# Optimization experiments

Hardware: AMD Instinct MI355X
Metric: run time of the kernel (lower is better)

Reference implementation:

```python
import jax, jax.numpy as jnp
import numpy as np

KAPPA = 10000.0
B_CONST = 0.5


def pe_matrix(L, dim):
    # pe[j,i] = sin(j/kappa^(i/dim)) for even i, cos(j/kappa^((i-1)/dim)) for odd i
    j = jnp.arange(L, dtype=jnp.float32)[:, None]
    i = jnp.arange(dim, dtype=jnp.float32)[None, :]
    even = (jnp.arange(dim) % 2 == 0)[None, :]
    expo = jnp.where(even, i, i - 1.0) / dim
    ang = j / (KAPPA ** expo)
    return jnp.where(even, jnp.sin(ang), jnp.cos(ang))  # [L, dim]


def setup_inputs() -> dict:
    key = jax.random.key(0)
    ks = jax.random.split(key, 6)
    B, N, L, d, n = 4, 8, 1024, 256, 3
    theta = jax.random.normal(ks[0], (B, N, L, d), dtype=jnp.float32)
    xi = jax.random.normal(ks[1], (B, N, L, n), dtype=jnp.float32)
    edge_attr = jax.random.normal(ks[2], (B, L, N * (N - 1) * 2), dtype=jnp.float32)
    s = 1.0 / np.sqrt(d)
    Wq = jax.random.normal(ks[3], (d, d), dtype=jnp.float32) * s
    Wk = jax.random.normal(ks[4], (d, d), dtype=jnp.float32) * s
    Wv = jax.random.normal(ks[5], (d, d), dtype=jnp.float32) * s
    return {"theta": theta, "xi": xi, "edge_attr": edge_attr, "Wq": Wq, "Wk": Wk, "Wv": Wv}


def reference(theta, xi, edge_attr, Wq, Wk, Wv):
    B, N, L, d = theta.shape
    n = xi.shape[-1]
    # positional encoding (dropout in eval mode = identity)
    theta = theta + pe_matrix(L, d)
    xi = xi + pe_matrix(L, n)
    edge_attr = edge_attr + pe_matrix(L, N * (N - 1) * 2)[None]

    causal = jnp.triu(jnp.ones((L, L), dtype=bool), 1)  # True above diagonal
    neg_inf = jnp.float32(-jnp.inf)

    # feature path: standard causal scaled-dot-product attention
    q = jnp.einsum('bnld,ed->bnle', theta, Wq)
    k = jnp.einsum('bnld,ed->bnle', theta, Wk)
    v = jnp.einsum('bnld,ed->bnle', theta, Wv)
    scores = jnp.einsum('bnqd,bnkd->bnqk', q, k) / jnp.sqrt(jnp.float32(d))
    scores = jnp.where(causal, neg_inf, scores)
    h_out = jnp.einsum('bnqk,bnkd->bnqd', jax.nn.softmax(scores, axis=-1), v)

    # equivariant path: pairwise squared-distance attention
    D = xi[:, :, :, None, :] - xi[:, :, None, :, :]  # [B,N,L,L,n]
    sq = jnp.sum(D * D, axis=-1)                     # [B,N,L,L]
    sq = jnp.where(causal, neg_inf, sq)
    beta = jax.nn.softmax(sq, axis=-1)
    mbeta = beta * (1.0 - jnp.eye(L, dtype=beta.dtype))  # zero the diagonal
    second = B_CONST * jnp.einsum('bnqk,bnkc->bnqc', mbeta, xi)
    third = B_CONST * jnp.sum(mbeta, axis=-1, keepdims=True) * xi
    x_out = xi + second - third

    return h_out, x_out, edge_attr
```

## Files before the change

kernel.cpp:

```cpp
#include <hip/hip_runtime.h>
#include <math.h>

#define L    1024
#define D    256
#define NCH  3
#define HEADS 32
#define EDIM 112
#define BATCH 4

typedef __bf16 bf8_t __attribute__((ext_vector_type(8)));
typedef float  f4_t  __attribute__((ext_vector_type(4)));

typedef __attribute__((address_space(1))) const void GVC;
typedef __attribute__((address_space(3))) void LDSV;

__device__ inline unsigned short f2bf(float x) {
    unsigned u = __float_as_uint(x);
    u += 0x7FFFu + ((u >> 16) & 1u);
    return (unsigned short)(u >> 16);
}
__device__ inline float bf2f(unsigned short h) {
    return __uint_as_float(((unsigned)h) << 16);
}

__global__ void prep_kernel(const float* __restrict__ edge, const float* __restrict__ xi,
                            const float* __restrict__ Wq, const float* __restrict__ Wk,
                            const float* __restrict__ Wv,
                            float* __restrict__ pe_d, float* __restrict__ eout,
                            float* __restrict__ xsb, unsigned short* __restrict__ whb)
{
    int idx = blockIdx.x * blockDim.x + threadIdx.x;
    if (idx < L * D) {
        int l = idx >> 8, i = idx & (D - 1);
        float expo = (float)(i & ~1) * (1.0f / (float)D);
        float ang = (float)l * __powf(10000.0f, -expo);
        pe_d[idx] = (i & 1) ? cosf(ang) : sinf(ang);
    } else if (idx < L * D + BATCH * L * EDIM) {
        int j = idx - L * D;
        int i = j % EDIM;
        int l = (j / EDIM) % L;
        float expo = (float)(i & ~1) * (1.0f / (float)EDIM);
        float ang = (float)l * __powf(10000.0f, -expo);
        eout[j] = edge[j] + ((i & 1) ? cosf(ang) : sinf(ang));
    } else if (idx < L * D + BATCH * L * EDIM + HEADS * L * NCH) {
        int j = idx - (L * D + BATCH * L * EDIM);
        int c = j % 3;
        int l = (j / 3) & (L - 1);
        float ang = (c == 2) ? (float)l * 0.0021544347f : (float)l;
        float pe = (c == 1) ? cosf(ang) : sinf(ang);
        xsb[j] = xi[j] + pe;
    } else {
        int j = idx - (L * D + BATCH * L * EDIM + HEADS * L * NCH);
        if (j < 3 * 8192) {
            int wsel = j >> 13;
            int t = j & 8191;
            int g = t >> 9, u = (t >> 4) & 31, rr = t & 15;
            const float* W = (wsel == 0) ? Wq : (wsel == 1) ? Wk : Wv;
            const float4* s = reinterpret_cast<const float4*>(&W[(size_t)(g * 16 + rr) * D + u * 8]);
            float4 a = s[0], b = s[1];
            float x[8] = {a.x, a.y, a.z, a.w, b.x, b.y, b.z, b.w};
            union { unsigned short us[8]; float4 f4; } hv;
            #pragma unroll
            for (int q = 0; q < 8; q++) hv.us[q] = f2bf(x[q]);
            *reinterpret_cast<float4*>(&whb[(size_t)wsel * 65536 + g * 4096 + u * 128 + rr * 8]) = hv.f4;
        }
    }
}

__global__ __launch_bounds__(512) void qkv_mfma(
    const float* __restrict__ theta, const float* __restrict__ pe_d,
    const unsigned short* __restrict__ whb,
    unsigned short* __restrict__ qh, unsigned short* __restrict__ ql,
    unsigned short* __restrict__ kh, unsigned short* __restrict__ vt)
{
    __shared__ __align__(16) unsigned short XsH[2][4096];
    __shared__ __align__(16) unsigned short XsL[2][4096];
    __shared__ __align__(16) unsigned short Ws[2][8192];

    int tid = threadIdx.x;
    int w = tid >> 6, lane = tid & 63;
    int quad = lane >> 4, l16 = lane & 15;
    int eh = w & 1;
    int xq = w >> 1;

    int b = blockIdx.x;
    int xcd = b & 7, r = b >> 3;
    int wsel = r % 3;
    int panel = (r / 3) * 8 + xcd;
    int rowBase = panel * 128;
    const unsigned short* wsrc = whb + (size_t)wsel * 65536;

    int sr = tid >> 2;
    int ks8 = (tid & 3) * 8;
    int cg = sr >> 4, cr = sr & 15, cu = tid & 3;
    int xoff = cg * 512 + cu * 128 + cr * 8;

    const float* tp_base = &theta[(size_t)(rowBase + sr) * D + ks8];
    const float* pp_base = &pe_d[(size_t)((rowBase + sr) & (L - 1)) * D + ks8];

    f4_t acc[16];
    #pragma unroll
    for (int i = 0; i < 16; i++) acc[i] = (f4_t){0.f, 0.f, 0.f, 0.f};

    auto stageW = [&](int kt, int buf) {
        #pragma unroll
        for (int j = 0; j < 2; j++) {
            int g = w * 2 + j;
            __builtin_amdgcn_global_load_lds(
                (GVC*)(wsrc + (size_t)g * 4096 + kt * 512 + lane * 8),
                (LDSV*)(Ws[buf] + g * 512), 16, 0, 0);
        }
    };
    auto loadX = [&](int kt, float* xv) {
        const float* tp = tp_base + kt * 32;
        const float* pp = pp_base + kt * 32;
        float4 t0 = reinterpret_cast<const float4*>(tp)[0];
        float4 t1 = reinterpret_cast<const float4*>(tp)[1];
        float4 p0 = reinterpret_cast<const float4*>(pp)[0];
        float4 p1 = reinterpret_cast<const float4*>(pp)[1];
        xv[0] = t0.x + p0.x; xv[1] = t0.y + p0.y; xv[2] = t0.z + p0.z; xv[3] = t0.w + p0.w;
        xv[4] = t1.x + p1.x; xv[5] = t1.y + p1.y; xv[6] = t1.z + p1.z; xv[7] = t1.w + p1.w;
    };
    auto convX = [&](const float* xv, int buf) {
        union { unsigned short us[8]; float4 f4; } h, lo;
        #pragma unroll
        for (int e = 0; e < 8; e++) {
            unsigned short hh = f2bf(xv[e]);
            h.us[e] = hh;
            lo.us[e] = f2bf(xv[e] - bf2f(hh));
        }
        *reinterpret_cast<float4*>(&XsH[buf][xoff]) = h.f4;
        *reinterpret_cast<float4*>(&XsL[buf][xoff]) = lo.f4;
    };

    {
        float xv[8];
        loadX(0, xv);
        convX(xv, 0);
        stageW(0, 0);
    }
    __syncthreads();

    #define FR(buf2d, g16) (*reinterpret_cast<const bf8_t*>(&(buf2d)[(g16) * 512 + quad * 128 + l16 * 8]))

    for (int kt = 0; kt < 8; kt++) {
        int buf = kt & 1;

        float xn[8];
        if (kt < 7) {
            stageW(kt + 1, buf ^ 1);
            loadX(kt + 1, xn);
        }
        __builtin_amdgcn_sched_barrier(0);

        bf8_t bxh[2], bxl[2];
        #pragma unroll
        for (int nx = 0; nx < 2; nx++) {
            bxh[nx] = FR(XsH[buf], xq * 2 + nx);
            bxl[nx] = FR(XsL[buf], xq * 2 + nx);
        }

        if (wsel < 2) {
            #pragma unroll
            for (int ne = 0; ne < 8; ne++) {
                bf8_t aw = FR(Ws[buf], eh * 8 + ne);
                #pragma unroll
                for (int nx = 0; nx < 2; nx++) {
                    acc[ne * 2 + nx] = __builtin_amdgcn_mfma_f32_16x16x32_bf16(aw, bxh[nx], acc[ne * 2 + nx], 0, 0, 0);
                    acc[ne * 2 + nx] = __builtin_amdgcn_mfma_f32_16x16x32_bf16(aw, bxl[nx], acc[ne * 2 + nx], 0, 0, 0);
                }
            }
        } else {
            #pragma unroll
            for (int ne = 0; ne < 8; ne++) {
                bf8_t bw = FR(Ws[buf], eh * 8 + ne);
                #pragma unroll
                for (int mx = 0; mx < 2; mx++) {
                    acc[mx * 8 + ne] = __builtin_amdgcn_mfma_f32_16x16x32_bf16(bxh[mx], bw, acc[mx * 8 + ne], 0, 0, 0);
                    acc[mx * 8 + ne] = __builtin_amdgcn_mfma_f32_16x16x32_bf16(bxl[mx], bw, acc[mx * 8 + ne], 0, 0, 0);
                }
            }
        }

        if (kt < 7) convX(xn, buf ^ 1);
        __syncthreads();
    }
    #undef FR

    if (wsel < 2) {
        float scale = (wsel == 0) ? 0.0625f : 1.0f;
        #pragma unroll
        for (int ne = 0; ne < 8; ne++) {
            #pragma unroll
            for (int nx = 0; nx < 2; nx++) {
                int e0 = eh * 128 + ne * 16 + quad * 4;
                size_t row = rowBase + xq * 32 + nx * 16 + l16;
                union { unsigned short us[4]; unsigned long long u; } ph, pl;
                #pragma unroll
                for (int rr = 0; rr < 4; rr++) {
                    float x = acc[ne * 2 + nx][rr] * scale;
                    unsigned short h = f2bf(x);
                    ph.us[rr] = h;
                    pl.us[rr] = f2bf(x - bf2f(h));
                }
                if (wsel == 0) {
                    *reinterpret_cast<unsigned long long*>(&qh[row * D + e0]) = ph.u;
                    *reinterpret_cast<unsigned long long*>(&ql[row * D + e0]) = pl.u;
                } else {
                    int e0s = e0 ^ ((l16 & 7) << 3);
                    *reinterpret_cast<unsigned long long*>(&kh[row * D + e0s]) = ph.u;
                }
            }
        }
    } else {
        #pragma unroll
        for (int mx = 0; mx < 2; mx++) {
            #pragma unroll
            for (int ne = 0; ne < 8; ne++) {
                int row0 = rowBase + xq * 32 + mx * 16 + quad * 4;
                int e = eh * 128 + ne * 16 + l16;
                int head = row0 >> 10, kb = (row0 & 1023) >> 5, kk = row0 & 31;
                union { unsigned short us[4]; unsigned long long u; } pk;
                #pragma unroll
                for (int rr = 0; rr < 4; rr++) pk.us[rr] = f2bf(acc[mx * 8 + ne][rr]);
                int us_sw = (e * 32 + kk) ^ (((e >> 1) & 3) << 3);
                *reinterpret_cast<unsigned long long*>(
                    &vt[((size_t)(head * 32 + kb)) * 8192 + us_sw]) = pk.u;
            }
        }
    }
}

__device__ __forceinline__ void stage_super(
    const unsigned short* kht, const unsigned short* vtt,
    unsigned short* Ks, unsigned short* Vs, int st, int buf, int w, int lane)
{
    #pragma unroll
    for (int j = 0; j < 2; j++) {
        int t = st * 2 + j;
        #pragma unroll
        for (int i = 0; i < 2; i++) {
            int ch = w * 2 + i;
            __builtin_amdgcn_global_load_lds(
                (GVC*)(kht + (size_t)t * 8192 + ch * 512 + lane * 8),
                (LDSV*)(Ks + buf * 16384 + j * 8192 + ch * 512), 16, 0, 0);
            __builtin_amdgcn_global_load_lds(
                (GVC*)(vtt + (size_t)t * 8192 + ch * 512 + lane * 8),
                (LDSV*)(Vs + buf * 16384 + j * 8192 + ch * 512), 16, 0, 0);
        }
    }
}

__global__ __launch_bounds__(512) __attribute__((amdgpu_waves_per_eu(2, 2)))
void attn_v10(
    const unsigned short* __restrict__ qh, const unsigned short* __restrict__ ql,
    const unsigned short* __restrict__ kh, const unsigned short* __restrict__ vt,
    float* __restrict__ hout)
{
    __shared__ __align__(16) unsigned short Ks[2 * 16384];
    __shared__ __align__(16) unsigned short Vs[2 * 16384];
    __shared__ __align__(16) unsigned short Pb[8][2][16 * 40];

    int tid = threadIdx.x;
    int w = tid >> 6, lane = tid & 63;
    int quad = lane >> 4, l16 = lane & 15;
    int b = blockIdx.x;
    int head = ((b & 7) << 2) + (b >> 6);
    int s = (b >> 3) & 7;
    int u = (w < 4) ? (4 * s + w) : (63 - 4 * s - (w - 4));
    int Ts = 32 - 2 * s;
    int nSup = Ts >> 1;
    int limS = u >> 2;
    size_t hb = (size_t)head * (L * D);
    const unsigned short* kht = kh + hb;
    const unsigned short* vtt = vt + (size_t)head * (32 * 8192);
    unsigned short* PwA = Pb[w][0];
    unsigned short* PwB = Pb[w][1];

    int q_g = u * 16 + l16;

    f4_t qfh[8], qfl[8];
    {
        const unsigned short* ph = qh + hb + (size_t)q_g * D + quad * 8;
        const unsigned short* pl = ql + hb + (size_t)q_g * D + quad * 8;
        #pragma unroll
        for (int c = 0; c < 8; c++) {
            qfh[c] = *reinterpret_cast<const f4_t*>(ph + c * 32);
            qfl[c] = *reinterpret_cast<const f4_t*>(pl + c * 32);
        }
    }
    #pragma unroll
    for (int c = 0; c < 8; c++) {
        asm volatile("" : "+v"(qfh[c]));
        asm volatile("" : "+v"(qfl[c]));
    }

    stage_super(kht, vtt, Ks, Vs, 0, 0, w, lane);

    f4_t acc[16];
    #pragma unroll
    for (int i = 0; i < 16; i++) acc[i] = (f4_t){0.f, 0.f, 0.f, 0.f};
    float mrun = -1e30f, lrun = 0.f;

    int xm = (l16 & 7) << 3;
    int vq = (quad * 8) ^ (((l16 >> 1) & 3) << 3);

    #pragma unroll 1
    for (int st = 0; st < nSup; st++) {
        asm volatile("s_waitcnt vmcnt(0)" ::: "memory");
        __builtin_amdgcn_s_barrier();
        __builtin_amdgcn_sched_barrier(0);
        int ns = (st + 1 < nSup) ? st + 1 : nSup - 1;
        stage_super(kht, vtt, Ks, Vs, ns, (st + 1) & 1, w, lane);

        if (st <= limS) {
            const unsigned short* Kb0 = Ks + (st & 1) * 16384;
            const unsigned short* Vb0 = Vs + (st & 1) * 16384;
            const unsigned short* Kb1 = Kb0 + 8192;
            const unsigned short* Vb1 = Vb0 + 8192;
            int kBase = st * 64;

            bf8_t kf0[8], kf1[8];
            #pragma unroll
            for (int c = 0; c < 8; c++) {
                int col = (quad * 8 + c * 32) ^ xm;
                kf0[c] = *reinterpret_cast<const bf8_t*>(&Kb0[l16 * 256 + col]);
                kf1[c] = *reinterpret_cast<const bf8_t*>(&Kb0[(16 + l16) * 256 + col]);
            }
            f4_t a0 = (f4_t){0.f,0.f,0.f,0.f}, a1 = (f4_t){0.f,0.f,0.f,0.f};
            f4_t a2 = (f4_t){0.f,0.f,0.f,0.f}, a3 = (f4_t){0.f,0.f,0.f,0.f};
            __builtin_amdgcn_s_setprio(1);
            #pragma unroll
            for (int c = 0; c < 8; c += 2) {
                a0 = __builtin_amdgcn_mfma_f32_16x16x32_bf16(kf0[c],     __builtin_bit_cast(bf8_t, qfh[c]),     a0, 0, 0, 0);
                a1 = __builtin_amdgcn_mfma_f32_16x16x32_bf16(kf0[c + 1], __builtin_bit_cast(bf8_t, qfh[c + 1]), a1, 0, 0, 0);
                a0 = __builtin_amdgcn_mfma_f32_16x16x32_bf16(kf0[c],     __builtin_bit_cast(bf8_t, qfl[c]),     a0, 0, 0, 0);
                a1 = __builtin_amdgcn_mfma_f32_16x16x32_bf16(kf0[c + 1], __builtin_bit_cast(bf8_t, qfl[c + 1]), a1, 0, 0, 0);
                a2 = __builtin_amdgcn_mfma_f32_16x16x32_bf16(kf1[c],     __builtin_bit_cast(bf8_t, qfh[c]),     a2, 0, 0, 0);
                a3 = __builtin_amdgcn_mfma_f32_16x16x32_bf16(kf1[c + 1], __builtin_bit_cast(bf8_t, qfh[c + 1]), a3, 0, 0, 0);
                a2 = __builtin_amdgcn_mfma_f32_16x16x32_bf16(kf1[c],     __builtin_bit_cast(bf8_t, qfl[c]),     a2, 0, 0, 0);
                a3 = __builtin_amdgcn_mfma_f32_16x16x32_bf16(kf1[c + 1], __builtin_bit_cast(bf8_t, qfl[c + 1]), a3, 0, 0, 0);
            }
            __builtin_amdgcn_s_setprio(0);
            f4_t scA[2];
            scA[0] = a0 + a1;
            scA[1] = a2 + a3;

            bf8_t kf2[8], kf3[8];
            #pragma unroll
            for (int c = 0; c < 8; c++) {
                int col = (quad * 8 + c * 32) ^ xm;
                kf2[c] = *reinterpret_cast<const bf8_t*>(&Kb1[l16 * 256 + col]);
                kf3[c] = *reinterpret_cast<const bf8_t*>(&Kb1[(16 + l16) * 256 + col]);
            }
            f4_t b0 = (f4_t){0.f,0.f,0.f,0.f}, b1 = (f4_t){0.f,0.f,0.f,0.f};
            f4_t b2 = (f4_t){0.f,0.f,0.f,0.f}, b3 = (f4_t){0.f,0.f,0.f,0.f};
            __builtin_amdgcn_s_setprio(1);
            #pragma unroll
            for (int c = 0; c < 8; c += 2) {
                b0 = __builtin_amdgcn_mfma_f32_16x16x32_bf16(kf2[c],     __builtin_bit_cast(bf8_t, qfh[c]),     b0, 0, 0, 0);
                b1 = __builtin_amdgcn_mfma_f32_16x16x32_bf16(kf2[c + 1], __builtin_bit_cast(bf8_t, qfh[c + 1]), b1, 0, 0, 0);
                b0 = __builtin_amdgcn_mfma_f32_16x16x32_bf16(kf2[c],     __builtin_bit_cast(bf8_t, qfl[c]),     b0, 0, 0, 0);
                b1 = __builtin_amdgcn_mfma_f32_16x16x32_bf16(kf2[c + 1], __builtin_bit_cast(bf8_t, qfl[c + 1]), b1, 0, 0, 0);
                b2 = __builtin_amdgcn_mfma_f32_16x16x32_bf16(kf3[c],     __builtin_bit_cast(bf8_t, qfh[c]),     b2, 0, 0, 0);
                b3 = __builtin_amdgcn_mfma_f32_16x16x32_bf16(kf3[c + 1], __builtin_bit_cast(bf8_t, qfh[c + 1]), b3, 0, 0, 0);
                b2 = __builtin_amdgcn_mfma_f32_16x16x32_bf16(kf3[c],     __builtin_bit_cast(bf8_t, qfl[c]),     b2, 0, 0, 0);
                b3 = __builtin_amdgcn_mfma_f32_16x16x32_bf16(kf3[c + 1], __builtin_bit_cast(bf8_t, qfl[c + 1]), b3, 0, 0, 0);
            }
            __builtin_amdgcn_s_setprio(0);
            f4_t scB[2];
            scB[0] = b0 + b1;
            scB[1] = b2 + b3;

            const unsigned short* vp0 = Vb0 + l16 * 32 + vq;
            const unsigned short* vp1 = Vb1 + l16 * 32 + vq;
            bf8_t vfA[8];
            #pragma unroll
            for (int dt = 0; dt < 8; dt++)
                vfA[dt] = *reinterpret_cast<const bf8_t*>(vp0 + dt * 512);

            float pvA[2][4], pvB[2][4];
            float tm = -1e30f;
            #pragma unroll
            for (int t = 0; t < 2; t++)
                #pragma unroll
                for (int rr = 0; rr < 4; rr++) {
                    int keyA = kBase + t * 16 + quad * 4 + rr;
                    int keyB = keyA + 32;
                    float svA = (keyA <= q_g) ? scA[t][rr] : -1e30f;
                    float svB = (keyB <= q_g) ? scB[t][rr] : -1e30f;
                    scA[t][rr] = svA;
                    scB[t][rr] = svB;
                    tm = fmaxf(tm, fmaxf(svA, svB));
                }
            tm = fmaxf(tm, __shfl_xor(tm, 16));
            tm = fmaxf(tm, __shfl_xor(tm, 32));
            bool grow = __any(tm > mrun);
            float mnew = fmaxf(mrun, tm);
            float alpha = grow ? __expf(mrun - mnew) : 1.0f;
            mrun = mnew;
            float ts = 0.f;
            #pragma unroll
            for (int t = 0; t < 2; t++)
                #pragma unroll
                for (int rr = 0; rr < 4; rr++) {
                    float pA = __expf(scA[t][rr] - mnew);
                    float pB = __expf(scB[t][rr] - mnew);
                    pvA[t][rr] = pA;
                    pvB[t][rr] = pB;
                    ts += pA + pB;
                }
            ts += __shfl_xor(ts, 16);
            ts += __shfl_xor(ts, 32);
            lrun = lrun * alpha + ts;

            #pragma unroll
            for (int t = 0; t < 2; t++) {
                union { unsigned short us[4]; unsigned long long uu; } pkA, pkB;
                #pragma unroll
                for (int rr = 0; rr < 4; rr++) {
                    pkA.us[rr] = f2bf(pvA[t][rr]);
                    pkB.us[rr] = f2bf(pvB[t][rr]);
                }
                *reinterpret_cast<unsigned long long*>(&PwA[l16 * 40 + t * 16 + quad * 4]) = pkA.uu;
                *reinterpret_cast<unsigned long long*>(&PwB[l16 * 40 + t * 16 + quad * 4]) = pkB.uu;
            }
            if (grow) {
                #pragma unroll
                for (int dt = 0; dt < 16; dt++) acc[dt] *= alpha;
            }
            asm volatile("s_waitcnt lgkmcnt(0)" ::: "memory");
            bf8_t pfA = *reinterpret_cast<const bf8_t*>(&PwA[l16 * 40 + quad * 8]);
            __builtin_amdgcn_s_setprio(1);
            #pragma unroll
            for (int dt = 0; dt < 8; dt++)
                acc[dt] = __builtin_amdgcn_mfma_f32_16x16x32_bf16(vfA[dt], pfA, acc[dt], 0, 0, 0);
            __builtin_amdgcn_s_setprio(0);
            bf8_t vfA2[8];
            #pragma unroll
            for (int dt = 0; dt < 8; dt++)
                vfA2[dt] = *reinterpret_cast<const bf8_t*>(vp0 + (8 + dt) * 512);
            __builtin_amdgcn_s_setprio(1);
            #pragma unroll
            for (int dt = 0; dt < 8; dt++)
                acc[8 + dt] = __builtin_amdgcn_mfma_f32_16x16x32_bf16(vfA2[dt], pfA, acc[8 + dt], 0, 0, 0);
            __builtin_amdgcn_s_setprio(0);
            bf8_t vfB[8];
            #pragma unroll
            for (int dt = 0; dt < 8; dt++)
                vfB[dt] = *reinterpret_cast<const bf8_t*>(vp1 + dt * 512);
            bf8_t pfB = *reinterpret_cast<const bf8_t*>(&PwB[l16 * 40 + quad * 8]);
            __builtin_amdgcn_s_setprio(1);
            #pragma unroll
            for (int dt = 0; dt < 8; dt++)
                acc[dt] = __builtin_amdgcn_mfma_f32_16x16x32_bf16(vfB[dt], pfB, acc[dt], 0, 0, 0);
            __builtin_amdgcn_s_setprio(0);
            bf8_t vfB2[8];
            #pragma unroll
            for (int dt = 0; dt < 8; dt++)
                vfB2[dt] = *reinterpret_cast<const bf8_t*>(vp1 + (8 + dt) * 512);
            __builtin_amdgcn_s_setprio(1);
            #pragma unroll
            for (int dt = 0; dt < 8; dt++)
                acc[8 + dt] = __builtin_amdgcn_mfma_f32_16x16x32_bf16(vfB2[dt], pfB, acc[8 + dt], 0, 0, 0);
            __builtin_amdgcn_s_setprio(0);
        }
    }

    float inv = 1.f / lrun;
    float* dst = hout + hb + (size_t)q_g * D + quad * 4;
    #pragma unroll
    for (int dt = 0; dt < 16; dt++) {
        float4 o = {acc[dt][0] * inv, acc[dt][1] * inv,
                    acc[dt][2] * inv, acc[dt][3] * inv};
        *reinterpret_cast<float4*>(dst + dt * 16) = o;
    }
}

__global__ __launch_bounds__(256) void equiv_kernel(
    const float* __restrict__ xsb, float* __restrict__ xout)
{
    __shared__ float xs[L * NCH];
    int head = blockIdx.y;
    int tid = threadIdx.x;
    const float4* src = reinterpret_cast<const float4*>(xsb + (size_t)head * L * NCH);
    #pragma unroll
    for (int it = 0; it < 3; it++)
        reinterpret_cast<float4*>(xs)[tid + it * 256] = src[tid + it * 256];
    __syncthreads();

    int w = tid >> 6, lane = tid & 63;
    int q = blockIdx.x * 4 + w;
    float xq0 = xs[q * 3 + 0], xq1 = xs[q * 3 + 1], xq2 = xs[q * 3 + 2];

    float m = 0.f;
    for (int k = lane; k < q; k += 64) {
        float d0 = xq0 - xs[k * 3 + 0];
        float d1 = xq1 - xs[k * 3 + 1];
        float d2 = xq2 - xs[k * 3 + 2];
        m = fmaxf(m, d0 * d0 + d1 * d1 + d2 * d2);
    }
    #pragma unroll
    for (int off = 1; off < 64; off <<= 1) m = fmaxf(m, __shfl_xor(m, off));

    float s0 = 0.f, s1 = 0.f, s2 = 0.f, sn = 0.f;
    for (int k = lane; k < q; k += 64) {
        float d0 = xq0 - xs[k * 3 + 0];
        float d1 = xq1 - xs[k * 3 + 1];
        float d2 = xq2 - xs[k * 3 + 2];
        float wgt = __expf(d0 * d0 + d1 * d1 + d2 * d2 - m);
        sn += wgt;
        s0 += wgt * xs[k * 3 + 0];
        s1 += wgt * xs[k * 3 + 1];
        s2 += wgt * xs[k * 3 + 2];
    }
    #pragma unroll
    for (int off = 1; off < 64; off <<= 1) {
        sn += __shfl_xor(sn, off);
        s0 += __shfl_xor(s0, off);
        s1 += __shfl_xor(s1, off);
        s2 += __shfl_xor(s2, off);
    }
    float Z = sn + __expf(-m);
    float inv = 0.5f / Z;
    if (lane == 0) {
        size_t ob = (size_t)head * L * NCH + (size_t)q * NCH;
        xout[ob + 0] = xq0 + inv * (s0 - sn * xq0);
        xout[ob + 1] = xq1 + inv * (s1 - sn * xq1);
        xout[ob + 2] = xq2 + inv * (s2 - sn * xq2);
    }
}

extern "C" void kernel_launch(void* const* d_in, const int* in_sizes, int n_in,
                              void* d_out, int out_size, void* d_ws, size_t ws_size,
                              hipStream_t stream)
{
    (void)in_sizes; (void)n_in; (void)out_size; (void)ws_size;
    const float* theta = (const float*)d_in[0];
    const float* xi    = (const float*)d_in[1];
    const float* edge  = (const float*)d_in[2];
    const float* Wq    = (const float*)d_in[3];
    const float* Wk    = (const float*)d_in[4];
    const float* Wv    = (const float*)d_in[5];

    float* out  = (float*)d_out;
    float* hout = out;
    float* xout = out + 8388608;
    float* eout = out + 8388608 + 98304;

    const size_t NE = 8388608;
    unsigned short* base = (unsigned short*)d_ws;
    unsigned short* qh  = base;
    unsigned short* ql  = base + NE;
    unsigned short* kh  = base + 2 * NE;
    unsigned short* vt  = base + 3 * NE;
    unsigned short* whb = base + 4 * NE;
    float* pe_d = (float*)(base + 4 * NE + 196608);
    float* xsb  = pe_d + L * D;

    prep_kernel<<<3296, 256, 0, stream>>>(edge, xi, Wq, Wk, Wv, pe_d, eout, xsb, whb);
    equiv_kernel<<<dim3(L / 4, HEADS), 256, 0, stream>>>(xsb, xout);
    qkv_mfma<<<768, 512, 0, stream>>>(theta, pe_d, whb, qh, ql, kh, vt);
    attn_v10<<<256, 512, 0, stream>>>(qh, ql, kh, vt, hout);
}
```

Before: 221.1 us.

## Deepen QKV projection pipeline to multi-stage prefetch with manual waitcnt barriers

```diff
diff --git a/kernel.cpp b/kernel.cpp
--- a/kernel.cpp
+++ b/kernel.cpp
@@ -67,15 +67,16 @@
     }
 }
 
-__global__ __launch_bounds__(512) void qkv_mfma(
+__global__ __launch_bounds__(512) __attribute__((amdgpu_waves_per_eu(2, 2)))
+void qkv_mfma(
     const float* __restrict__ theta, const float* __restrict__ pe_d,
     const unsigned short* __restrict__ whb,
     unsigned short* __restrict__ qh, unsigned short* __restrict__ ql,
     unsigned short* __restrict__ kh, unsigned short* __restrict__ vt)
 {
-    __shared__ __align__(16) unsigned short XsH[2][4096];
-    __shared__ __align__(16) unsigned short XsL[2][4096];
-    __shared__ __align__(16) unsigned short Ws[2][8192];
+    __shared__ __align__(16) unsigned short XsH[3][4096];
+    __shared__ __align__(16) unsigned short XsL[3][4096];
+    __shared__ __align__(16) unsigned short Ws[4][8192];
 
     int tid = threadIdx.x;
     int w = tid >> 6, lane = tid & 63;
@@ -90,13 +91,13 @@
     int rowBase = panel * 128;
     const unsigned short* wsrc = whb + (size_t)wsel * 65536;
 
-    int sr = tid >> 2;
-    int ks8 = (tid & 3) * 8;
-    int cg = sr >> 4, cr = sr & 15, cu = tid & 3;
-    int xoff = cg * 512 + cu * 128 + cr * 8;
-
-    const float* tp_base = &theta[(size_t)(rowBase + sr) * D + ks8];
-    const float* pp_base = &pe_d[(size_t)((rowBase + sr) & (L - 1)) * D + ks8];
+    int cr = tid & 15;
+    int cu = (tid >> 4) & 3;
+    int sr = w * 16 + cr;
+    int xoff = w * 512 + cu * 128 + cr * 8;
+
+    const float* tp_base = &theta[(size_t)(rowBase + sr) * D + cu * 8];
+    const float* pp_base = &pe_d[(size_t)((rowBase + sr) & (L - 1)) * D + cu * 8];
 
     f4_t acc[16];
     #pragma unroll
@@ -111,17 +112,17 @@
                 (LDSV*)(Ws[buf] + g * 512), 16, 0, 0);
         }
     };
-    auto loadX = [&](int kt, float* xv) {
+    auto loadX = [&](int kt, float4* tv) {
         const float* tp = tp_base + kt * 32;
         const float* pp = pp_base + kt * 32;
-        float4 t0 = reinterpret_cast<const float4*>(tp)[0];
-        float4 t1 = reinterpret_cast<const float4*>(tp)[1];
-        float4 p0 = reinterpret_cast<const float4*>(pp)[0];
-        float4 p1 = reinterpret_cast<const float4*>(pp)[1];
-        xv[0] = t0.x + p0.x; xv[1] = t0.y + p0.y; xv[2] = t0.z + p0.z; xv[3] = t0.w + p0.w;
-        xv[4] = t1.x + p1.x; xv[5] = t1.y + p1.y; xv[6] = t1.z + p1.z; xv[7] = t1.w + p1.w;
+        tv[0] = reinterpret_cast<const float4*>(tp)[0];
+        tv[1] = reinterpret_cast<const float4*>(tp + 4)[0];
+        tv[2] = reinterpret_cast<const float4*>(pp)[0];
+        tv[3] = reinterpret_cast<const float4*>(pp + 4)[0];
     };
-    auto convX = [&](const float* xv, int buf) {
+    auto convX = [&](const float4* tv, int buf) {
+        float xv[8] = {tv[0].x + tv[2].x, tv[0].y + tv[2].y, tv[0].z + tv[2].z, tv[0].w + tv[2].w,
+                       tv[1].x + tv[3].x, tv[1].y + tv[3].y, tv[1].z + tv[3].z, tv[1].w + tv[3].w};
         union { unsigned short us[8]; float4 f4; } h, lo;
         #pragma unroll
         for (int e = 0; e < 8; e++) {
@@ -133,37 +134,41 @@
         *reinterpret_cast<float4*>(&XsL[buf][xoff]) = lo.f4;
     };
 
-    {
-        float xv[8];
-        loadX(0, xv);
-        convX(xv, 0);
-        stageW(0, 0);
-    }
-    __syncthreads();
+    float4 t0v[4], t1v[4], tcur[4];
+    loadX(0, t0v);
+    loadX(1, t1v);
+    stageW(0, 0);
+    stageW(1, 1);
+    stageW(2, 2);
+    loadX(2, tcur);
+    convX(t0v, 0);
+    convX(t1v, 1);
+    asm volatile("s_waitcnt vmcnt(8)" ::: "memory");
+    asm volatile("s_waitcnt lgkmcnt(0)" ::: "memory");
+    __builtin_amdgcn_s_barrier();
 
     #define FR(buf2d, g16) (*reinterpret_cast<const bf8_t*>(&(buf2d)[(g16) * 512 + quad * 128 + l16 * 8]))
 
-    for (int kt = 0; kt < 8; kt++) {
-        int buf = kt & 1;
-
-        float xn[8];
-        if (kt < 7) {
-            stageW(kt + 1, buf ^ 1);
-            loadX(kt + 1, xn);
-        }
+    #pragma unroll
+    for (int i = 0; i < 8; i++) {
+        int wb = i & 3;
+        int xb = i % 3;
+
+        float4 tn[4];
+        loadX((i + 3) & 7, tn);
+        stageW((i + 3) & 7, (i + 3) & 3);
         __builtin_amdgcn_sched_barrier(0);
 
         bf8_t bxh[2], bxl[2];
         #pragma unroll
         for (int nx = 0; nx < 2; nx++) {
-            bxh[nx] = FR(XsH[buf], xq * 2 + nx);
-            bxl[nx] = FR(XsL[buf], xq * 2 + nx);
-        }
-
+            bxh[nx] = FR(XsH[xb], xq * 2 + nx);
+            bxl[nx] = FR(XsL[xb], xq * 2 + nx);
+        }
         if (wsel < 2) {
             #pragma unroll
             for (int ne = 0; ne < 8; ne++) {
-                bf8_t aw = FR(Ws[buf], eh * 8 + ne);
+                bf8_t aw = FR(Ws[wb], eh * 8 + ne);
                 #pragma unroll
                 for (int nx = 0; nx < 2; nx++) {
                     acc[ne * 2 + nx] = __builtin_amdgcn_mfma_f32_16x16x32_bf16(aw, bxh[nx], acc[ne * 2 + nx], 0, 0, 0);
@@ -173,7 +178,7 @@
         } else {
             #pragma unroll
             for (int ne = 0; ne < 8; ne++) {
-                bf8_t bw = FR(Ws[buf], eh * 8 + ne);
+                bf8_t bw = FR(Ws[wb], eh * 8 + ne);
                 #pragma unroll
                 for (int mx = 0; mx < 2; mx++) {
                     acc[mx * 8 + ne] = __builtin_amdgcn_mfma_f32_16x16x32_bf16(bxh[mx], bw, acc[mx * 8 + ne], 0, 0, 0);
@@ -182,8 +187,13 @@
             }
         }
 
-        if (kt < 7) convX(xn, buf ^ 1);
-        __syncthreads();
+        asm volatile("s_waitcnt vmcnt(6)" ::: "memory");
+        convX(tcur, (i + 2) % 3);
+        #pragma unroll
+        for (int j = 0; j < 4; j++) tcur[j] = tn[j];
+
+        asm volatile("s_waitcnt lgkmcnt(0)" ::: "memory");
+        __builtin_amdgcn_s_barrier();
     }
     #undef FR
 
```

After: 235.1 us. 6.3% more time.

## Stage full X panel once in LDS and compute Q, K, V per block

Applied to the files above, without the earlier changes.

```diff
diff --git a/kernel.cpp b/kernel.cpp
--- a/kernel.cpp
+++ b/kernel.cpp
@@ -67,15 +67,17 @@
     }
 }
 
-__global__ __launch_bounds__(512) void qkv_mfma(
+__device__ inline int xswz(int b) { return b ^ (((b >> 8) & 3) << 5); }
+
+__global__ __launch_bounds__(512) __attribute__((amdgpu_waves_per_eu(2, 2)))
+void qkv_mfma(
     const float* __restrict__ theta, const float* __restrict__ pe_d,
     const unsigned short* __restrict__ whb,
     unsigned short* __restrict__ qh, unsigned short* __restrict__ ql,
     unsigned short* __restrict__ kh, unsigned short* __restrict__ vt)
 {
-    __shared__ __align__(16) unsigned short XsH[2][4096];
-    __shared__ __align__(16) unsigned short XsL[2][4096];
-    __shared__ __align__(16) unsigned short Ws[2][8192];
+    __shared__ __align__(16) unsigned short XsH[32768];
+    __shared__ __align__(16) unsigned short XsL[32768];
 
     int tid = threadIdx.x;
     int w = tid >> 6, lane = tid & 63;
@@ -83,149 +85,119 @@
     int eh = w & 1;
     int xq = w >> 1;
 
-    int b = blockIdx.x;
-    int xcd = b & 7, r = b >> 3;
-    int wsel = r % 3;
-    int panel = (r / 3) * 8 + xcd;
+    int panel = blockIdx.x;
     int rowBase = panel * 128;
-    const unsigned short* wsrc = whb + (size_t)wsel * 65536;
-
-    int sr = tid >> 2;
-    int ks8 = (tid & 3) * 8;
-    int cg = sr >> 4, cr = sr & 15, cu = tid & 3;
-    int xoff = cg * 512 + cu * 128 + cr * 8;
-
-    const float* tp_base = &theta[(size_t)(rowBase + sr) * D + ks8];
-    const float* pp_base = &pe_d[(size_t)((rowBase + sr) & (L - 1)) * D + ks8];
-
-    f4_t acc[16];
-    #pragma unroll
-    for (int i = 0; i < 16; i++) acc[i] = (f4_t){0.f, 0.f, 0.f, 0.f};
-
-    auto stageW = [&](int kt, int buf) {
+
+    {
+        int lrow = lane >> 5;
+        int ucol = lane & 31;
+        int ktc = ucol >> 2, quc = ucol & 3;
         #pragma unroll
-        for (int j = 0; j < 2; j++) {
-            int g = w * 2 + j;
-            __builtin_amdgcn_global_load_lds(
-                (GVC*)(wsrc + (size_t)g * 4096 + kt * 512 + lane * 8),
-                (LDSV*)(Ws[buf] + g * 512), 16, 0, 0);
-        }
-    };
-    auto loadX = [&](int kt, float* xv) {
-        const float* tp = tp_base + kt * 32;
-        const float* pp = pp_base + kt * 32;
-        float4 t0 = reinterpret_cast<const float4*>(tp)[0];
-        float4 t1 = reinterpret_cast<const float4*>(tp)[1];
-        float4 p0 = reinterpret_cast<const float4*>(pp)[0];
-        float4 p1 = reinterpret_cast<const float4*>(pp)[1];
-        xv[0] = t0.x + p0.x; xv[1] = t0.y + p0.y; xv[2] = t0.z + p0.z; xv[3] = t0.w + p0.w;
-        xv[4] = t1.x + p1.x; xv[5] = t1.y + p1.y; xv[6] = t1.z + p1.z; xv[7] = t1.w + p1.w;
-    };
-    auto convX = [&](const float* xv, int buf) {
-        union { unsigned short us[8]; float4 f4; } h, lo;
+        for (int j = 0; j < 8; j++) {
+            int rr = j * 2 + lrow;
+            int row = rowBase + w * 16 + rr;
+            const float* tp = &theta[(size_t)row * D + ucol * 8];
+            const float* pp = &pe_d[(size_t)(row & (L - 1)) * D + ucol * 8];
+            float4 t0 = reinterpret_cast<const float4*>(tp)[0];
+            float4 t1 = reinterpret_cast<const float4*>(tp)[1];
+            float4 p0 = reinterpret_cast<const float4*>(pp)[0];
+            float4 p1 = reinterpret_cast<const float4*>(pp)[1];
+            float xv[8] = {t0.x + p0.x, t0.y + p0.y, t0.z + p0.z, t0.w + p0.w,
+                           t1.x + p1.x, t1.y + p1.y, t1.z + p1.z, t1.w + p1.w};
+            union { unsigned short us[8]; float4 f4; } h, lo;
+            #pragma unroll
+            for (int e = 0; e < 8; e++) {
+                unsigned short hh = f2bf(xv[e]);
+                h.us[e] = hh;
+                lo.us[e] = f2bf(xv[e] - bf2f(hh));
+            }
+            int B = xswz(ktc * 8192 + w * 1024 + quc * 256 + rr * 16);
+            *reinterpret_cast<float4*>(reinterpret_cast<char*>(XsH) + B) = h.f4;
+            *reinterpret_cast<float4*>(reinterpret_cast<char*>(XsL) + B) = lo.f4;
+        }
+    }
+    __syncthreads();
+
+    for (int wsel = 0; wsel < 3; wsel++) {
+        const unsigned short* wsrc = whb + (size_t)wsel * 65536;
+
+        f4_t acc[16];
         #pragma unroll
-        for (int e = 0; e < 8; e++) {
-            unsigned short hh = f2bf(xv[e]);
-            h.us[e] = hh;
-            lo.us[e] = f2bf(xv[e] - bf2f(hh));
-        }
-        *reinterpret_cast<float4*>(&XsH[buf][xoff]) = h.f4;
-        *reinterpret_cast<float4*>(&XsL[buf][xoff]) = lo.f4;
-    };
-
-    {
-        float xv[8];
-        loadX(0, xv);
-        convX(xv, 0);
-        stageW(0, 0);
-    }
-    __syncthreads();
-
-    #define FR(buf2d, g16) (*reinterpret_cast<const bf8_t*>(&(buf2d)[(g16) * 512 + quad * 128 + l16 * 8]))
-
-    for (int kt = 0; kt < 8; kt++) {
-        int buf = kt & 1;
-
-        float xn[8];
-        if (kt < 7) {
-            stageW(kt + 1, buf ^ 1);
-            loadX(kt + 1, xn);
-        }
-        __builtin_amdgcn_sched_barrier(0);
-
-        bf8_t bxh[2], bxl[2];
+        for (int i = 0; i < 16; i++) acc[i] = (f4_t){0.f, 0.f, 0.f, 0.f};
+
         #pragma unroll
-        for (int nx = 0; nx < 2; nx++) {
-            bxh[nx] = FR(XsH[buf], xq * 2 + nx);
-            bxl[nx] = FR(XsL[buf], xq * 2 + nx);
+        for (int kt = 0; kt < 8; kt++) {
+            bf8_t wf[8];
+            #pragma unroll
+            for (int ne = 0; ne < 8; ne++)
+                wf[ne] = *reinterpret_cast<const bf8_t*>(
+                    wsrc + (size_t)(eh * 8 + ne) * 4096 + kt * 512 + lane * 8);
+            bf8_t bxh[2], bxl[2];
+            #pragma unroll
+            for (int nx = 0; nx < 2; nx++) {
+                int B = xswz(kt * 8192 + (xq * 2 + nx) * 1024 + quad * 256 + l16 * 16);
+                bxh[nx] = *reinterpret_cast<const bf8_t*>(reinterpret_cast<char*>(XsH) + B);
+                bxl[nx] = *reinterpret_cast<const bf8_t*>(reinterpret_cast<char*>(XsL) + B);
+            }
+            if (wsel != 2) {
+                #pragma unroll
+                for (int ne = 0; ne < 8; ne++)
+                    #pragma unroll
+                    for (int nx = 0; nx < 2; nx++) {
+                        acc[ne * 2 + nx] = __builtin_amdgcn_mfma_f32_16x16x32_bf16(wf[ne], bxh[nx], acc[ne * 2 + nx], 0, 0, 0);
+                        acc[ne * 2 + nx] = __builtin_amdgcn_mfma_f32_16x16x32_bf16(wf[ne], bxl[nx], acc[ne * 2 + nx], 0, 0, 0);
+                    }
+            } else {
+                #pragma unroll
+                for (int ne = 0; ne < 8; ne++)
+                    #pragma unroll
+                    for (int mx = 0; mx < 2; mx++) {
+                        acc[mx * 8 + ne] = __builtin_amdgcn_mfma_f32_16x16x32_bf16(bxh[mx], wf[ne], acc[mx * 8 + ne], 0, 0, 0);
+                        acc[mx * 8 + ne] = __builtin_amdgcn_mfma_f32_16x16x32_bf16(bxl[mx], wf[ne], acc[mx * 8 + ne], 0, 0, 0);
+                    }
+            }
         }
 
         if (wsel < 2) {
+            float scale = (wsel == 0) ? 0.0625f : 1.0f;
             #pragma unroll
             for (int ne = 0; ne < 8; ne++) {
-                bf8_t aw = FR(Ws[buf], eh * 8 + ne);
                 #pragma unroll
                 for (int nx = 0; nx < 2; nx++) {
-                    acc[ne * 2 + nx] = __builtin_amdgcn_mfma_f32_16x16x32_bf16(aw, bxh[nx], acc[ne * 2 + nx], 0, 0, 0);
-                    acc[ne * 2 + nx] = __builtin_amdgcn_mfma_f32_16x16x32_bf16(aw, bxl[nx], acc[ne * 2 + nx], 0, 0, 0);
+                    int e0 = eh * 128 + ne * 16 + quad * 4;
+                    size_t row = rowBase + xq * 32 + nx * 16 + l16;
+                    union { unsigned short us[4]; unsigned long long u; } ph, pl;
+                    #pragma unroll
+                    for (int rr = 0; rr < 4; rr++) {
+                        float x = acc[ne * 2 + nx][rr] * scale;
+                        unsigned short h = f2bf(x);
+                        ph.us[rr] = h;
+                        pl.us[rr] = f2bf(x - bf2f(h));
+                    }
+                    if (wsel == 0) {
+                        *reinterpret_cast<unsigned long long*>(&qh[row * D + e0]) = ph.u;
+                        *reinterpret_cast<unsigned long long*>(&ql[row * D + e0]) = pl.u;
+                    } else {
+                        int e0s = e0 ^ ((l16 & 7) << 3);
+                        *reinterpret_cast<unsigned long long*>(&kh[row * D + e0s]) = ph.u;
+                    }
                 }
             }
         } else {
             #pragma unroll
-            for (int ne = 0; ne < 8; ne++) {
-                bf8_t bw = FR(Ws[buf], eh * 8 + ne);
-                #pragma unroll
-                for (int mx = 0; mx < 2; mx++) {
-                    acc[mx * 8 + ne] = __builtin_amdgcn_mfma_f32_16x16x32_bf16(bxh[mx], bw, acc[mx * 8 + ne], 0, 0, 0);
-                    acc[mx * 8 + ne] = __builtin_amdgcn_mfma_f32_16x16x32_bf16(bxl[mx], bw, acc[mx * 8 + ne], 0, 0, 0);
+            for (int mx = 0; mx < 2; mx++) {
+                #pragma unroll
+                for (int ne = 0; ne < 8; ne++) {
+                    int row0 = rowBase + xq * 32 + mx * 16 + quad * 4;
+                    int e = eh * 128 + ne * 16 + l16;
+                    int head = row0 >> 10, kb = (row0 & 1023) >> 5, kk = row0 & 31;
+                    union { unsigned short us[4]; unsigned long long u; } pk;
+                    #pragma unroll
+                    for (int rr = 0; rr < 4; rr++) pk.us[rr] = f2bf(acc[mx * 8 + ne][rr]);
+                    int us_sw = (e * 32 + kk) ^ (((e >> 1) & 3) << 3);
+                    *reinterpret_cast<unsigned long long*>(
+                        &vt[((size_t)(head * 32 + kb)) * 8192 + us_sw]) = pk.u;
                 }
-            }
-        }
-
-        if (kt < 7) convX(xn, buf ^ 1);
-        __syncthreads();
-    }
-    #undef FR
-
-    if (wsel < 2) {
-        float scale = (wsel == 0) ? 0.0625f : 1.0f;
-        #pragma unroll
-        for (int ne = 0; ne < 8; ne++) {
-            #pragma unroll
-            for (int nx = 0; nx < 2; nx++) {
-                int e0 = eh * 128 + ne * 16 + quad * 4;
-                size_t row = rowBase + xq * 32 + nx * 16 + l16;
-                union { unsigned short us[4]; unsigned long long u; } ph, pl;
-                #pragma unroll
-                for (int rr = 0; rr < 4; rr++) {
-                    float x = acc[ne * 2 + nx][rr] * scale;
-                    unsigned short h = f2bf(x);
-                    ph.us[rr] = h;
-                    pl.us[rr] = f2bf(x - bf2f(h));
-                }
-                if (wsel == 0) {
-                    *reinterpret_cast<unsigned long long*>(&qh[row * D + e0]) = ph.u;
-                    *reinterpret_cast<unsigned long long*>(&ql[row * D + e0]) = pl.u;
-                } else {
-                    int e0s = e0 ^ ((l16 & 7) << 3);
-                    *reinterpret_cast<unsigned long long*>(&kh[row * D + e0s]) = ph.u;
-                }
-            }
-        }
-    } else {
-        #pragma unroll
-        for (int mx = 0; mx < 2; mx++) {
-            #pragma unroll
-            for (int ne = 0; ne < 8; ne++) {
-                int row0 = rowBase + xq * 32 + mx * 16 + quad * 4;
-                int e = eh * 128 + ne * 16 + l16;
-                int head = row0 >> 10, kb = (row0 & 1023) >> 5, kk = row0 & 31;
-                union { unsigned short us[4]; unsigned long long u; } pk;
-                #pragma unroll
-                for (int rr = 0; rr < 4; rr++) pk.us[rr] = f2bf(acc[mx * 8 + ne][rr]);
-                int us_sw = (e * 32 + kk) ^ (((e >> 1) & 3) << 3);
-                *reinterpret_cast<unsigned long long*>(
-                    &vt[((size_t)(head * 32 + kb)) * 8192 + us_sw]) = pk.u;
             }
         }
     }
@@ -560,6 +532,6 @@
 
     prep_kernel<<<3296, 256, 0, stream>>>(edge, xi, Wq, Wk, Wv, pe_d, eout, xsb, whb);
     equiv_kernel<<<dim3(L / 4, HEADS), 256, 0, stream>>>(xsb, xout);
-    qkv_mfma<<<768, 512, 0, stream>>>(theta, pe_d, whb, qh, ql, kh, vt);
+    qkv_mfma<<<256, 512, 0, stream>>>(theta, pe_d, whb, qh, ql, kh, vt);
     attn_v10<<<256, 512, 0, stream>>>(qh, ql, kh, vt, hout);
 }
```

After: 234.0 us. 5.8% more time.
